# Optimization experiments

Hardware: AMD Instinct MI355X
Metric: run time of the kernel (lower is better)

The kernel has to match this reference:

```python
import jax, jax.numpy as jnp
import numpy as np

EMBED_DIM = 1024
NUM_HEADS = 16
HEAD_DIM = EMBED_DIM // NUM_HEADS


def setup_inputs() -> dict:
    key = jax.random.key(0)
    ks = jax.random.split(key, 5)
    B, N, C = 2, 2048, EMBED_DIM
    s = 0.02
    return {
        "x": jax.random.normal(ks[0], (B, N, C), dtype=jnp.float32),
        "w_qkv": jax.random.normal(ks[1], (C, 3 * C), dtype=jnp.float32) * s,
        "b_qkv": jax.random.normal(ks[2], (3 * C,), dtype=jnp.float32) * s,
        "w_proj": jax.random.normal(ks[3], (C, C), dtype=jnp.float32) * s,
        "b_proj": jax.random.normal(ks[4], (C,), dtype=jnp.float32) * s,
    }


def reference(x, w_qkv, b_qkv, w_proj, b_proj):
    B, N, C = x.shape
    H, D = NUM_HEADS, C // NUM_HEADS
    scale = D ** -0.5
    qkv = x @ w_qkv + b_qkv                      # [B,N,3C]
    qkv = qkv.reshape(B, N, 3, H, D).transpose(2, 0, 3, 1, 4)  # [3,B,H,N,D]
    q, k, v = qkv[0] * scale, qkv[1], qkv[2]
    attn = jnp.einsum("bhnd,bhmd->bhnm", q, k)   # [B,H,N,N]
    attn = jax.nn.softmax(attn, axis=-1)
    out = jnp.einsum("bhnm,bhmd->bhnd", attn, v)  # [B,H,N,D]
    out = out.transpose(0, 2, 1, 3).reshape(B, N, C)
    return out @ w_proj + b_proj
```

## Files before the change

kernel.cpp:

```cpp
#include <hip/hip_runtime.h>

typedef short bf16x8 __attribute__((ext_vector_type(8)));
typedef float f32x4 __attribute__((ext_vector_type(4)));
typedef float f32x16 __attribute__((ext_vector_type(16)));
typedef unsigned short ushort8 __attribute__((ext_vector_type(8)));
typedef unsigned short ushort4v __attribute__((ext_vector_type(4)));
typedef unsigned int uint4v __attribute__((ext_vector_type(4)));
typedef unsigned short u16;

__device__ inline u16 f2bf(float f) {
  unsigned int u = __float_as_uint(f);
  u += 0x7fffu + ((u >> 16) & 1u);
  return (u16)(u >> 16);
}

__device__ inline unsigned cvt_pk_bf16(float lo, float hi2) {
  unsigned r;
  asm("v_cvt_pk_bf16_f32 %0, %1, %2" : "=v"(r) : "v"(lo), "v"(hi2));
  return r;
}

__device__ inline void perm32swap(unsigned& a, unsigned& b) {
  asm("v_permlane32_swap_b32 %0, %1" : "+v"(a), "+v"(b));
}

__device__ inline void gload_lds16(const u16* g, u16* l) {
  __builtin_amdgcn_global_load_lds(
      (const __attribute__((address_space(1))) unsigned int*)g,
      (__attribute__((address_space(3))) unsigned int*)l, 16, 0, 0);
}

__global__ __launch_bounds__(256) void cvt_bf16(const float* __restrict__ in,
                                                u16* __restrict__ out, int n) {
  int i = (blockIdx.x * 256 + threadIdx.x) * 8;
  if (i >= n) return;
  float4 a = *(const float4*)(in + i);
  float4 b = *(const float4*)(in + i + 4);
  ushort8 o;
  o[0] = f2bf(a.x); o[1] = f2bf(a.y); o[2] = f2bf(a.z); o[3] = f2bf(a.w);
  o[4] = f2bf(b.x); o[5] = f2bf(b.y); o[6] = f2bf(b.z); o[7] = f2bf(b.w);
  *(ushort8*)(out + i) = o;
}

__global__ __launch_bounds__(256) void trans_w(const float* __restrict__ W,
                                               u16* __restrict__ Wt, int K, int N) {
  const int k0 = blockIdx.x * 64, n0 = blockIdx.y * 64;
  const int tx = threadIdx.x & 63, ty = threadIdx.x >> 6;
  __shared__ float t[64][65];
#pragma unroll
  for (int i = 0; i < 16; ++i) {
    int r = i * 4 + ty;
    t[r][tx] = W[(size_t)(k0 + r) * N + n0 + tx];
  }
  __syncthreads();
#pragma unroll
  for (int i = 0; i < 16; ++i) {
    int r = i * 4 + ty;
    Wt[(size_t)(n0 + r) * K + k0 + tx] = f2bf(t[tx][r]);
  }
}

template <int MODE>
__global__ __launch_bounds__(256) void gemm_bt(
    const u16* __restrict__ A, const u16* __restrict__ Bt, int M, int N, int K,
    const float* __restrict__ bias, float* __restrict__ outF,
    u16* __restrict__ Qb, u16* __restrict__ Kb, u16* __restrict__ Vb) {
  const int bm = blockIdx.x * 128;
  const int bn = blockIdx.y * 128;
  const int tid = threadIdx.x;
  const int wid = tid >> 6;
  const int lr = tid & 15;
  const int lg = (tid >> 4) & 3;
  const int wr = wid >> 1, wc = wid & 1;

  __shared__ u16 smem[32768];
  u16* Ab0 = smem;
  u16* Ab1 = smem + 8192;
  u16* Bb0 = smem + 16384;
  u16* Bb1 = smem + 24576;

  f32x4 acc[4][4] = {};

  const int rowi = tid >> 3;
  const int sslot = ((tid & 7) ^ (rowi & 7)) * 8;
  const u16* Ag = A + (size_t)bm * K;
  const u16* Bg = Bt + (size_t)bn * K;
  const int nkt = K >> 6;

  auto stage = [&](u16* Ad, u16* Bd, int kt) {
    const int kof = kt << 6;
#pragma unroll
    for (int i = 0; i < 4; ++i) {
      const int row = i * 32 + rowi;
      gload_lds16(Ag + (size_t)row * K + kof + sslot, Ad + (i * 32 + wid * 8) * 64);
      gload_lds16(Bg + (size_t)row * K + kof + sslot, Bd + (i * 32 + wid * 8) * 64);
    }
  };

  stage(Ab0, Bb0, 0);
  __syncthreads();

  for (int kt = 0; kt < nkt; ++kt) {
    const int p = kt & 1;
    const char* Ard = (const char*)(p ? Ab1 : Ab0);
    const char* Brd = (const char*)(p ? Bb1 : Bb0);
    bf16x8 af[4], bfr[4];
#pragma unroll
    for (int t = 0; t < 4; ++t) {
      const int ra = wr * 64 + t * 16 + lr;
      const int rb = wc * 64 + t * 16 + lr;
      af[t] = *(const bf16x8*)(Ard + ra * 128 + ((lg * 16) ^ ((ra & 7) << 4)));
      bfr[t] = *(const bf16x8*)(Brd + rb * 128 + ((lg * 16) ^ ((rb & 7) << 4)));
    }
    if (kt + 1 < nkt) stage(p ? Ab0 : Ab1, p ? Bb0 : Bb1, kt + 1);
    __builtin_amdgcn_s_setprio(1);
#pragma unroll
    for (int mt = 0; mt < 4; ++mt)
#pragma unroll
      for (int nt = 0; nt < 4; ++nt)
        acc[mt][nt] = __builtin_amdgcn_mfma_f32_16x16x32_bf16(
            af[mt], bfr[nt], acc[mt][nt], 0, 0, 0);
    __builtin_amdgcn_s_setprio(0);
#pragma unroll
    for (int t = 0; t < 4; ++t) {
      const int ra = wr * 64 + t * 16 + lr;
      const int rb = wc * 64 + t * 16 + lr;
      af[t] = *(const bf16x8*)(Ard + ra * 128 + ((64 + lg * 16) ^ ((ra & 7) << 4)));
      bfr[t] = *(const bf16x8*)(Brd + rb * 128 + ((64 + lg * 16) ^ ((rb & 7) << 4)));
    }
    __builtin_amdgcn_s_setprio(1);
#pragma unroll
    for (int mt = 0; mt < 4; ++mt)
#pragma unroll
      for (int nt = 0; nt < 4; ++nt)
        acc[mt][nt] = __builtin_amdgcn_mfma_f32_16x16x32_bf16(
            af[mt], bfr[nt], acc[mt][nt], 0, 0, 0);
    __builtin_amdgcn_s_setprio(0);
    __syncthreads();
  }

  if (MODE == 1) {
#pragma unroll
    for (int mt = 0; mt < 4; ++mt) {
      const int row0 = bm + wr * 64 + mt * 16 + lg * 4;
#pragma unroll
      for (int nt = 0; nt < 4; ++nt) {
        const int col = bn + wc * 64 + nt * 16 + lr;
        const float bv = bias[col];
#pragma unroll
        for (int r = 0; r < 4; ++r)
          outF[(size_t)(row0 + r) * N + col] = acc[mt][nt][r] + bv;
      }
    }
    return;
  }

  u16* T = smem;
  const int which = bn >> 10;

  if (which == 2) {
#pragma unroll
    for (int nt = 0; nt < 4; ++nt) {
      const int cl = wc * 64 + nt * 16 + lr;
      const float bv = bias[bn + cl];
#pragma unroll
      for (int mt = 0; mt < 4; ++mt) {
        const int rlb = wr * 128 + mt * 32 + lg * 8;
        ushort4v pk;
#pragma unroll
        for (int r = 0; r < 4; ++r) pk[r] = f2bf(acc[mt][nt][r] + bv);
        *(ushort4v*)((char*)T + cl * 256 + (rlb ^ ((cl & 7) << 4))) = pk;
      }
    }
  } else {
    const float sc = (which == 0) ? 0.18033688f : 1.0f;
#pragma unroll
    for (int mt = 0; mt < 4; ++mt) {
      const int rl0 = wr * 64 + mt * 16 + lg * 4;
#pragma unroll
      for (int nt = 0; nt < 4; ++nt) {
        const int cl = wc * 64 + nt * 16 + lr;
        const float bv = bias[bn + cl];
#pragma unroll
        for (int r = 0; r < 4; ++r) {
          const int rl = rl0 + r;
          *(u16*)((char*)T + rl * 256 + ((cl * 2) ^ ((rl & 7) << 4))) =
              f2bf((acc[mt][nt][r] + bv) * sc);
        }
      }
    }
  }
  __syncthreads();

  const int b = bm >> 11;
  const int nbase = bm & 2047;
  if (which == 0) {
#pragma unroll
    for (int i = 0; i < 8; ++i) {
      const int c = i * 256 + tid;
      const int rl = c >> 4, dch = c & 15;
      uint4v v =
          *(const uint4v*)((const char*)T + rl * 256 + ((dch * 16) ^ ((rl & 7) << 4)));
      const int bh = b * 16 + (bn >> 6) + (dch >> 3);
      *(uint4v*)(Qb + ((size_t)bh * 2048 + nbase + rl) * 64 + (dch & 7) * 8) = v;
    }
  } else if (which == 1) {
#pragma unroll
    for (int i = 0; i < 8; ++i) {
      const int c = i * 256 + tid;
      const int lane = c & 63, s = (c >> 6) & 7, ktl = (c >> 9) & 1, hl = c >> 10;
      const int lq = lane & 31, hi2 = lane >> 5;
      const int rl = ktl * 64 + (s & 1) * 32 + lq;
      const int cc = hl * 128 + (s >> 1) * 32 + hi2 * 16;
      uint4v v = *(const uint4v*)((const char*)T + rl * 256 + (cc ^ ((rl & 7) << 4)));
      const int bh = b * 16 + ((bn & 1023) >> 6) + hl;
      const int kt2 = (nbase >> 6) + ktl;
      *(uint4v*)(Kb + ((((size_t)bh * 32 + kt2) * 8 + s) * 64 + lane) * 8) = v;
    }
  } else {
#pragma unroll
    for (int i = 0; i < 8; ++i) {
      const int c = i * 256 + tid;
      const int lane = c & 63, s = (c >> 6) & 7, ktl = (c >> 9) & 1, hl = c >> 10;
      const int lq = lane & 31, hi2 = lane >> 5;
      const int cl = hl * 64 + (s & 1) * 32 + lq;
      const int cc = ktl * 128 + (s >> 1) * 32 + hi2 * 16;
      uint4v v = *(const uint4v*)((const char*)T + cl * 256 + (cc ^ ((cl & 7) << 4)));
      const int bh = b * 16 + ((bn & 1023) >> 6) + hl;
      const int kt2 = (nbase >> 6) + ktl;
      *(uint4v*)(Vb + ((((size_t)bh * 32 + kt2) * 8 + s) * 64 + lane) * 8) = v;
    }
  }
}

__global__ __launch_bounds__(256, 3) void flash_attn9(const u16* __restrict__ Qb,
                                                      const u16* __restrict__ Kp,
                                                      const u16* __restrict__ Vp,
                                                      u16* __restrict__ AO) {
  const int bh = blockIdx.x & 31;
  const int qt = blockIdx.x >> 5;
  const int tid = threadIdx.x;
  const int w = tid >> 6;
  const int qw = w & 1;
  const int half = w >> 1;
  const int lane = tid & 63;
  const int lq = lane & 31;
  const int hi = lane >> 5;
  const int q0 = qt * 64 + qw * 32;

  __shared__ float mrg[2][64][33];

  const u16* Qg = Qb + ((size_t)bh * 2048 + q0 + lq) * 64 + 8 * hi;
  bf16x8 qf[4];
#pragma unroll
  for (int t = 0; t < 4; ++t) qf[t] = *(const bf16x8*)(Qg + 16 * t);

  const u16* Kg = Kp + (size_t)bh * (32 * 4096) + lane * 8;
  const u16* Vg = Vp + (size_t)bh * (32 * 4096) + lane * 8;

  f32x16 ot0 = {}, ot1 = {};
  float lacc[8] = {};

  const int kt0 = half * 16, kt1 = kt0 + 16;

  bf16x8 kbuf[8], vbuf[8];
#pragma unroll
  for (int s = 0; s < 8; ++s)
    kbuf[s] = *(const bf16x8*)(Kg + (size_t)kt0 * 4096 + s * 512);

  for (int kt = kt0; kt < kt1; ++kt) {
#pragma unroll
    for (int s = 0; s < 8; ++s)
      vbuf[s] = *(const bf16x8*)(Vg + (size_t)kt * 4096 + s * 512);

    f32x16 sa = {}, sb = {};
    __builtin_amdgcn_s_setprio(1);
#pragma unroll
    for (int t = 0; t < 4; ++t) {
      sa = __builtin_amdgcn_mfma_f32_32x32x16_bf16(kbuf[2 * t], qf[t], sa, 0, 0, 0);
      sb = __builtin_amdgcn_mfma_f32_32x32x16_bf16(kbuf[2 * t + 1], qf[t], sb, 0, 0, 0);
    }
    __builtin_amdgcn_s_setprio(0);

    if (kt + 1 < kt1) {
#pragma unroll
      for (int s = 0; s < 8; ++s)
        kbuf[s] = *(const bf16x8*)(Kg + (size_t)(kt + 1) * 4096 + s * 512);
    }

#pragma unroll
    for (int r = 0; r < 16; ++r) {
      sa[r] = __builtin_amdgcn_exp2f(sa[r]);
      sb[r] = __builtin_amdgcn_exp2f(sb[r]);
    }
#pragma unroll
    for (int r = 0; r < 8; ++r)
      lacc[r] += (sa[r] + sa[r + 8]) + (sb[r] + sb[r + 8]);

    unsigned Ua[8], Ub[8];
#pragma unroll
    for (int s = 0; s < 4; ++s)
#pragma unroll
      for (int m2 = 0; m2 < 2; ++m2) {
        Ua[s * 2 + m2] = cvt_pk_bf16(sa[4 * s + 2 * m2], sa[4 * s + 2 * m2 + 1]);
        Ub[s * 2 + m2] = cvt_pk_bf16(sb[4 * s + 2 * m2], sb[4 * s + 2 * m2 + 1]);
      }
    bf16x8 pfrag[4];
#pragma unroll
    for (int t = 0; t < 4; ++t) {
      const unsigned* U = (t < 2) ? Ua : Ub;
      const int tt = t & 1;
      unsigned w0 = U[(2 * tt) * 2 + 0], w2 = U[(2 * tt + 1) * 2 + 0];
      unsigned w1 = U[(2 * tt) * 2 + 1], w3 = U[(2 * tt + 1) * 2 + 1];
      perm32swap(w0, w2);
      perm32swap(w1, w3);
      uint4v uu = {w0, w1, w2, w3};
      pfrag[t] = __builtin_bit_cast(bf16x8, uu);
    }

    __builtin_amdgcn_s_setprio(1);
#pragma unroll
    for (int t = 0; t < 4; ++t) {
      ot0 = __builtin_amdgcn_mfma_f32_32x32x16_bf16(vbuf[2 * t], pfrag[t], ot0, 0, 0, 0);
      ot1 = __builtin_amdgcn_mfma_f32_32x32x16_bf16(vbuf[2 * t + 1], pfrag[t], ot1, 0, 0, 0);
    }
    __builtin_amdgcn_s_setprio(0);
  }

  float lsum = ((lacc[0] + lacc[1]) + (lacc[2] + lacc[3])) +
               ((lacc[4] + lacc[5]) + (lacc[6] + lacc[7]));
  lsum += __shfl_xor(lsum, 32, 64);

  float* mp = &mrg[qw][lane][0];
  if (half == 1) {
#pragma unroll
    for (int r = 0; r < 16; ++r) mp[r] = ot0[r];
#pragma unroll
    for (int r = 0; r < 16; ++r) mp[16 + r] = ot1[r];
    mp[32] = lsum;
  }
  __syncthreads();
  if (half == 1) return;

  const float inv = 1.0f / (lsum + mp[32]);
#pragma unroll
  for (int r = 0; r < 16; ++r) ot0[r] = (ot0[r] + mp[r]) * inv;
#pragma unroll
  for (int r = 0; r < 16; ++r) ot1[r] = (ot1[r] + mp[16 + r]) * inv;

  const int b = bh >> 4, h = bh & 15;
  u16* Ao = AO + ((size_t)(b * 2048 + q0 + lq)) * 1024 + h * 64;
#pragma unroll
  for (int s = 0; s < 4; ++s) {
    {
      const int d = 8 * s + 4 * hi;
      ushort4v pk;
#pragma unroll
      for (int i = 0; i < 4; ++i) pk[i] = f2bf(ot0[4 * s + i]);
      *(ushort4v*)(Ao + d) = pk;
    }
    {
      const int d = 32 + 8 * s + 4 * hi;
      ushort4v pk;
#pragma unroll
      for (int i = 0; i < 4; ++i) pk[i] = f2bf(ot1[4 * s + i]);
      *(ushort4v*)(Ao + d) = pk;
    }
  }
}

extern "C" void kernel_launch(void* const* d_in, const int* in_sizes, int n_in,
                              void* d_out, int out_size, void* d_ws, size_t ws_size,
                              hipStream_t stream) {
  const float* x = (const float*)d_in[0];
  const float* w_qkv = (const float*)d_in[1];
  const float* b_qkv = (const float*)d_in[2];
  const float* w_proj = (const float*)d_in[3];
  const float* b_proj = (const float*)d_in[4];
  float* out = (float*)d_out;

  char* ws = (char*)d_ws;
  u16* xb = (u16*)(ws);
  u16* wqT = (u16*)(ws + (8ull << 20));
  u16* wpT = (u16*)(ws + (14ull << 20));
  u16* Qb = (u16*)(ws + (16ull << 20));
  u16* Kp = (u16*)(ws + (24ull << 20));
  u16* Vp = (u16*)(ws + (32ull << 20));
  u16* AO = (u16*)(ws + (40ull << 20));

  cvt_bf16<<<dim3(2048), dim3(256), 0, stream>>>(x, xb, 4194304);
  trans_w<<<dim3(16, 48), dim3(256), 0, stream>>>(w_qkv, wqT, 1024, 3072);
  trans_w<<<dim3(16, 16), dim3(256), 0, stream>>>(w_proj, wpT, 1024, 1024);
  gemm_bt<0><<<dim3(32, 24), dim3(256), 0, stream>>>(xb, wqT, 4096, 3072, 1024,
                                                     b_qkv, nullptr, Qb, Kp, Vp);
  flash_attn9<<<dim3(1024), dim3(256), 0, stream>>>(Qb, Kp, Vp, AO);
  gemm_bt<1><<<dim3(32, 8), dim3(256), 0, stream>>>(AO, wpT, 4096, 1024, 1024,
                                                    b_proj, out, nullptr, nullptr,
                                                    nullptr);
}
```

Measured before the change: 114.0 us.

## Share K/V tiles across four query waves via double-buffered LDS staging

The attention kernel stops splitting the key range across wave pairs with a shared-memory merge. Instead each block of four waves now covers 128 queries and iterates over all 32 key tiles. K and V tiles are staged through double-buffered LDS with direct global-to-LDS loads and shared by all four waves, which cuts redundant global/L2 traffic. The trade-offs are a block-wide barrier every iteration, half as many blocks (512), and fewer resident blocks per CU under the new launch bounds.

```diff
diff --git a/kernel.cpp b/kernel.cpp
--- a/kernel.cpp
+++ b/kernel.cpp
@@ -233,60 +233,66 @@
   }
 }
 
-__global__ __launch_bounds__(256, 3) void flash_attn9(const u16* __restrict__ Qb,
-                                                      const u16* __restrict__ Kp,
-                                                      const u16* __restrict__ Vp,
-                                                      u16* __restrict__ AO) {
+__global__ __launch_bounds__(256, 2) void flash_attn10(const u16* __restrict__ Qb,
+                                                       const u16* __restrict__ Kp,
+                                                       const u16* __restrict__ Vp,
+                                                       u16* __restrict__ AO) {
   const int bh = blockIdx.x & 31;
   const int qt = blockIdx.x >> 5;
   const int tid = threadIdx.x;
   const int w = tid >> 6;
-  const int qw = w & 1;
-  const int half = w >> 1;
   const int lane = tid & 63;
   const int lq = lane & 31;
   const int hi = lane >> 5;
-  const int q0 = qt * 64 + qw * 32;
-
-  __shared__ float mrg[2][64][33];
+  const int q0 = qt * 128 + w * 32;
+
+  __shared__ u16 Kld[2][4096];
+  __shared__ u16 Vld[2][4096];
 
   const u16* Qg = Qb + ((size_t)bh * 2048 + q0 + lq) * 64 + 8 * hi;
   bf16x8 qf[4];
 #pragma unroll
   for (int t = 0; t < 4; ++t) qf[t] = *(const bf16x8*)(Qg + 16 * t);
 
-  const u16* Kg = Kp + (size_t)bh * (32 * 4096) + lane * 8;
-  const u16* Vg = Vp + (size_t)bh * (32 * 4096) + lane * 8;
+  const u16* Kg = Kp + (size_t)bh * (32 * 4096);
+  const u16* Vg = Vp + (size_t)bh * (32 * 4096);
 
   f32x16 ot0 = {}, ot1 = {};
   float lacc[8] = {};
 
-  const int kt0 = half * 16, kt1 = kt0 + 16;
-
-  bf16x8 kbuf[8], vbuf[8];
-#pragma unroll
-  for (int s = 0; s < 8; ++s)
-    kbuf[s] = *(const bf16x8*)(Kg + (size_t)kt0 * 4096 + s * 512);
-
-  for (int kt = kt0; kt < kt1; ++kt) {
+  auto stage = [&](int p, int kt) {
+    const size_t src = (size_t)kt * 4096;
+    gload_lds16(Kg + src + tid * 8, &Kld[p][tid * 8]);
+    gload_lds16(Kg + src + 2048 + tid * 8, &Kld[p][2048 + tid * 8]);
+    gload_lds16(Vg + src + tid * 8, &Vld[p][tid * 8]);
+    gload_lds16(Vg + src + 2048 + tid * 8, &Vld[p][2048 + tid * 8]);
+  };
+
+  stage(0, 0);
+  __syncthreads();
+
+  for (int kt = 0; kt < 32; ++kt) {
+    const int p = kt & 1;
+    if (kt < 31) stage(p ^ 1, kt + 1);
+
+    bf16x8 kf[8];
 #pragma unroll
     for (int s = 0; s < 8; ++s)
-      vbuf[s] = *(const bf16x8*)(Vg + (size_t)kt * 4096 + s * 512);
+      kf[s] = *(const bf16x8*)&Kld[p][s * 512 + lane * 8];
 
     f32x16 sa = {}, sb = {};
     __builtin_amdgcn_s_setprio(1);
 #pragma unroll
     for (int t = 0; t < 4; ++t) {
-      sa = __builtin_amdgcn_mfma_f32_32x32x16_bf16(kbuf[2 * t], qf[t], sa, 0, 0, 0);
-      sb = __builtin_amdgcn_mfma_f32_32x32x16_bf16(kbuf[2 * t + 1], qf[t], sb, 0, 0, 0);
+      sa = __builtin_amdgcn_mfma_f32_32x32x16_bf16(kf[2 * t], qf[t], sa, 0, 0, 0);
+      sb = __builtin_amdgcn_mfma_f32_32x32x16_bf16(kf[2 * t + 1], qf[t], sb, 0, 0, 0);
     }
     __builtin_amdgcn_s_setprio(0);
 
-    if (kt + 1 < kt1) {
-#pragma unroll
-      for (int s = 0; s < 8; ++s)
-        kbuf[s] = *(const bf16x8*)(Kg + (size_t)(kt + 1) * 4096 + s * 512);
-    }
+    bf16x8 vf[8];
+#pragma unroll
+    for (int s = 0; s < 8; ++s)
+      vf[s] = *(const bf16x8*)&Vld[p][s * 512 + lane * 8];
 
 #pragma unroll
     for (int r = 0; r < 16; ++r) {
@@ -321,32 +327,18 @@
     __builtin_amdgcn_s_setprio(1);
 #pragma unroll
     for (int t = 0; t < 4; ++t) {
-      ot0 = __builtin_amdgcn_mfma_f32_32x32x16_bf16(vbuf[2 * t], pfrag[t], ot0, 0, 0, 0);
-      ot1 = __builtin_amdgcn_mfma_f32_32x32x16_bf16(vbuf[2 * t + 1], pfrag[t], ot1, 0, 0, 0);
+      ot0 = __builtin_amdgcn_mfma_f32_32x32x16_bf16(vf[2 * t], pfrag[t], ot0, 0, 0, 0);
+      ot1 = __builtin_amdgcn_mfma_f32_32x32x16_bf16(vf[2 * t + 1], pfrag[t], ot1, 0, 0, 0);
     }
     __builtin_amdgcn_s_setprio(0);
+
+    __syncthreads();
   }
 
   float lsum = ((lacc[0] + lacc[1]) + (lacc[2] + lacc[3])) +
                ((lacc[4] + lacc[5]) + (lacc[6] + lacc[7]));
   lsum += __shfl_xor(lsum, 32, 64);
-
-  float* mp = &mrg[qw][lane][0];
-  if (half == 1) {
-#pragma unroll
-    for (int r = 0; r < 16; ++r) mp[r] = ot0[r];
-#pragma unroll
-    for (int r = 0; r < 16; ++r) mp[16 + r] = ot1[r];
-    mp[32] = lsum;
-  }
-  __syncthreads();
-  if (half == 1) return;
-
-  const float inv = 1.0f / (lsum + mp[32]);
-#pragma unroll
-  for (int r = 0; r < 16; ++r) ot0[r] = (ot0[r] + mp[r]) * inv;
-#pragma unroll
-  for (int r = 0; r < 16; ++r) ot1[r] = (ot1[r] + mp[16 + r]) * inv;
+  const float inv = 1.0f / lsum;
 
   const int b = bh >> 4, h = bh & 15;
   u16* Ao = AO + ((size_t)(b * 2048 + q0 + lq)) * 1024 + h * 64;
@@ -356,14 +348,14 @@
       const int d = 8 * s + 4 * hi;
       ushort4v pk;
 #pragma unroll
-      for (int i = 0; i < 4; ++i) pk[i] = f2bf(ot0[4 * s + i]);
+      for (int i = 0; i < 4; ++i) pk[i] = f2bf(ot0[4 * s + i] * inv);
       *(ushort4v*)(Ao + d) = pk;
     }
     {
       const int d = 32 + 8 * s + 4 * hi;
       ushort4v pk;
 #pragma unroll
-      for (int i = 0; i < 4; ++i) pk[i] = f2bf(ot1[4 * s + i]);
+      for (int i = 0; i < 4; ++i) pk[i] = f2bf(ot1[4 * s + i] * inv);
       *(ushort4v*)(Ao + d) = pk;
     }
   }
@@ -393,7 +385,7 @@
   trans_w<<<dim3(16, 16), dim3(256), 0, stream>>>(w_proj, wpT, 1024, 1024);
   gemm_bt<0><<<dim3(32, 24), dim3(256), 0, stream>>>(xb, wqT, 4096, 3072, 1024,
                                                      b_qkv, nullptr, Qb, Kp, Vp);
-  flash_attn9<<<dim3(1024), dim3(256), 0, stream>>>(Qb, Kp, Vp, AO);
+  flash_attn10<<<dim3(512), dim3(256), 0, stream>>>(Qb, Kp, Vp, AO);
   gemm_bt<1><<<dim3(32, 8), dim3(256), 0, stream>>>(AO, wpT, 4096, 1024, 1024,
                                                     b_proj, out, nullptr, nullptr,
                                                     nullptr);
```

After: 108.5 us. -4.9%, faster.
